# Kernel tuning notes

Measured on AMD Instinct MI355X. Metric: run time of the kernel, lower is better.

## Reference

```python
import jax, jax.numpy as jnp
import numpy as np

B, N, D, QM, QP, NP, T = 16, 900, 256, 4, 4, 6, 4


def setup_inputs() -> dict:
    key = jax.random.key(0)
    ks = jax.random.split(key, 12)
    return {
        "motion_query": jax.random.normal(ks[0], (B, N, D), jnp.float32),
        "plan_query": jax.random.normal(ks[1], (B, NP, D), jnp.float32),
        "ego_status_feature": jax.random.normal(ks[2], (B, D), jnp.float32),
        "motion_queue": jax.random.normal(ks[3], (B, QM, N, D), jnp.float32),
        "plan_queue": jax.random.normal(ks[4], (B, QP, NP, D), jnp.float32),
        "ego_status_queue": jax.random.normal(ks[5], (B, QP, D), jnp.float32),
        "period": jax.random.randint(ks[6], (B, QM), 0, 4, jnp.int32),
        "mask": jax.random.bernoulli(ks[7], 0.9, (B,)),
        "temp_anchor_embed_forstate": jax.random.normal(ks[8], (B, N, T, D), jnp.float32),
        "temp_mask_forstate": jax.random.bernoulli(ks[9], 0.5, (B, N, T)),
        "ego_temp_anchor_embed_forstate": jax.random.normal(ks[10], (B, 1, T, D), jnp.float32),
        "ego_temp_mask_forstate": jax.random.bernoulli(ks[11], 0.5, (B, 1, T)),
    }


def reference(motion_query, plan_query, ego_status_feature, motion_queue,
              plan_queue, ego_status_queue, period, mask,
              temp_anchor_embed_forstate, temp_mask_forstate,
              ego_temp_anchor_embed_forstate, ego_temp_mask_forstate):
    sg = jax.lax.stop_gradient
    # --- masked queue reset: for batch rows with mask==False, overwrite every
    # queue entry with the (detached) current value and zero the period ---
    reset = ~mask  # [B]
    mq = jnp.where(reset[:, None, None, None], sg(motion_query)[:, None], motion_queue)
    pq = jnp.where(reset[:, None, None, None], sg(plan_query)[:, None], plan_queue)
    eq = jnp.where(reset[:, None, None], sg(ego_status_feature)[:, None], ego_status_queue)
    per = jnp.where(reset[:, None], 0, period)

    # --- temporal window: T == 4, so both branches take the simple slice ---
    mm = temp_mask_forstate[..., :-1]            # [B, N, T-1]
    me = temp_anchor_embed_forstate[..., :-1, :]  # [B, N, T-1, D]
    pm = ego_temp_mask_forstate[..., :-1]         # [B, 1, T-1]
    pe = ego_temp_anchor_embed_forstate[..., :-1, :]  # [B, 1, T-1, D]

    # --- propagate plan embed forward over masked prefix ---
    any_flag = jnp.any(pm)
    all_true = jnp.all(pm, axis=(-2, -1))                # [B]
    m1 = pm[:, 0, :]                                     # [B, T-1] (Np == 1)
    first_false = jnp.argmin(m1, axis=-1)                # [B] index of first False
    Tm1 = pm.shape[-1]
    # embed at first-False slot (else branch) vs last-frame ego embed (all-True)
    repl_else = jnp.take_along_axis(pe, first_false[:, None, None, None], axis=2)[:, :, 0, :]
    repl_all = ego_temp_anchor_embed_forstate[:, :, -1, :]
    repl = jnp.where(all_true[:, None, None], repl_all, repl_else)  # [B, 1, D]
    j = jnp.arange(Tm1)
    overwrite = all_true[:, None] | (j[None, :] < first_false[:, None])  # [B, T-1]
    pe = jnp.where(any_flag & overwrite[:, None, :, None], repl[:, :, None, :], pe)

    return (mq, pq, eq, per,
            mm.swapaxes(1, 2), me.swapaxes(1, 2),
            pm.swapaxes(1, 2), pe.swapaxes(1, 2))
```

## Files before the change

### kernel.cpp

```cpp
#include <hip/hip_runtime.h>
#include <stdint.h>

namespace {
constexpr int Bn = 16, Nn = 900, Dn = 256, QMn = 4, QPn = 4, NPn = 6, Tn = 4;

constexpr int SZ_MQ  = Bn * QMn * Nn * Dn;
constexpr int SZ_PQ  = Bn * QPn * NPn * Dn;
constexpr int SZ_EQ  = Bn * QPn * Dn;
constexpr int SZ_PER = Bn * QMn;
constexpr int SZ_MM  = Bn * (Tn - 1) * Nn;
constexpr int SZ_ME  = Bn * (Tn - 1) * Nn * Dn;
constexpr int SZ_PM  = Bn * (Tn - 1);
constexpr int SZ_PE  = Bn * (Tn - 1) * Dn;

constexpr int OFF_MQ  = 0;
constexpr int OFF_PQ  = OFF_MQ + SZ_MQ;
constexpr int OFF_EQ  = OFF_PQ + SZ_PQ;
constexpr int OFF_PER = OFF_EQ + SZ_EQ;
constexpr int OFF_MM  = OFF_PER + SZ_PER;
constexpr int OFF_ME  = OFF_MM + SZ_MM;
constexpr int OFF_PM  = OFF_ME + SZ_ME;
constexpr int OFF_PE  = OFF_PM + SZ_PM;
constexpr int TOTAL   = OFF_PE + SZ_PE;
}

using u16 = unsigned short;

__device__ __forceinline__ float bits_to_f(unsigned u) {
    return __builtin_bit_cast(float, u);
}

__device__ int detect_float_mode(const void* p) {
    const unsigned* w = (const unsigned*)p;
    int cnt = 0;
#pragma unroll
    for (int i = 0; i < 32; ++i) {
        unsigned ex = (w[i] >> 7) & 0xFFu;
        cnt += (ex >= 120u && ex <= 133u) ? 1 : 0;
    }
    return (cnt >= 16) ? 1 : 0;
}

enum { BM_I32 = 0, BM_U8 = 1, BM_BF16 = 2, BM_F32 = 3 };
__device__ int detect_bool_mode(const void* p) {
    const unsigned* w = (const unsigned*)p;
    unsigned orw = 0, or_even = 0;
    bool hw_ok = true, u8_ok = true;
#pragma unroll
    for (int i = 0; i < 64; ++i) {
        unsigned x = w[i];
        orw |= x;
        unsigned lo = x & 0xFFFFu, hi = x >> 16;
        hw_ok = hw_ok && (lo == 0u || lo == 0x3F80u) && (hi == 0u || hi == 0x3F80u);
        or_even |= lo;
        u8_ok = u8_ok && ((x & 0xFEFEFEFEu) == 0u);
    }
    if (orw <= 1u) return BM_I32;
    if (hw_ok)     return (or_even == 0u) ? BM_F32 : BM_BF16;
    if (u8_ok)     return BM_U8;
    return BM_I32;
}

__device__ __forceinline__ bool get_bool(const void* p, int i, int m) {
    if (m == BM_I32) return ((const int*)p)[i] != 0;
    if (m == BM_U8)  return ((const unsigned char*)p)[i] != 0;
    if (m == BM_BF16) return ((const u16*)p)[i] != 0;
    return ((const unsigned*)p)[i] != 0;
}

__device__ int detect_period_mode(const void* p) {
    const unsigned* w = (const unsigned*)p;
    unsigned orw = 0, or_even = 0;
    bool hw_ok = true;
#pragma unroll
    for (int i = 0; i < 16; ++i) {
        unsigned x = w[i];
        orw |= x;
        unsigned lo = x & 0xFFFFu, hi = x >> 16;
        bool lo_ok = (lo == 0u || lo == 0x3F80u || lo == 0x4000u || lo == 0x4040u);
        bool hi_ok = (hi == 0u || hi == 0x3F80u || hi == 0x4000u || hi == 0x4040u);
        hw_ok = hw_ok && lo_ok && hi_ok;
        or_even |= lo;
    }
    if (orw <= 3u) return 0;
    if (hw_ok && or_even == 0u) return 2;
    return 1;
}

__device__ __forceinline__ float get_period_f(const void* p, int i, int m) {
    if (m == 0) return (float)((const int*)p)[i];
    if (m == 1) return bits_to_f((unsigned)((const u16*)p)[i] << 16);
    return ((const float*)p)[i];
}

__device__ __forceinline__ void load8f(const void* base, int e, int fm,
                                       float4& A, float4& B) {
    if (fm == 0) {
        const float* f = (const float*)base + e;
        A = reinterpret_cast<const float4*>(f)[0];
        B = reinterpret_cast<const float4*>(f)[1];
    } else {
        const int4 r = *reinterpret_cast<const int4*>((const u16*)base + e);
        unsigned x;
        x = (unsigned)r.x; A.x = bits_to_f(x << 16); A.y = bits_to_f(x & 0xFFFF0000u);
        x = (unsigned)r.y; A.z = bits_to_f(x << 16); A.w = bits_to_f(x & 0xFFFF0000u);
        x = (unsigned)r.z; B.x = bits_to_f(x << 16); B.y = bits_to_f(x & 0xFFFF0000u);
        x = (unsigned)r.w; B.z = bits_to_f(x << 16); B.w = bits_to_f(x & 0xFFFF0000u);
    }
}

__global__ __launch_bounds__(256) void state_queue_kernel(
    const void* __restrict__ motion_query,
    const void* __restrict__ plan_query,
    const void* __restrict__ ego_status_feature,
    const void* __restrict__ motion_queue,
    const void* __restrict__ plan_queue,
    const void* __restrict__ ego_status_queue,
    const void* __restrict__ period,
    const void* __restrict__ mask,
    const void* __restrict__ temp_anchor,
    const void* __restrict__ temp_mask,
    const void* __restrict__ ego_anchor,
    const void* __restrict__ ego_mask,
    float* __restrict__ out)
{
    __shared__ int s_modes[3];
    if (threadIdx.x == 0) {
        s_modes[0] = detect_float_mode(motion_query);
        s_modes[1] = detect_bool_mode(temp_mask);
        s_modes[2] = detect_period_mode(period);
    }
    __syncthreads();
    const int fm = s_modes[0];
    const int bm = s_modes[1];
    const int pmode = s_modes[2];

    const int pack = blockIdx.x * blockDim.x + threadIdx.x;
    const int idx = pack * 8;
    if (idx >= TOTAL) return;

    float4 A, B;

    if (idx < OFF_PQ) {
        const int e = idx - OFF_MQ;
        const int d = e & (Dn - 1);
        const unsigned row = (unsigned)(e >> 8);
        const unsigned bq = row / (unsigned)Nn;
        const unsigned n = row - bq * (unsigned)Nn;
        const unsigned b = bq >> 2;
        const bool reset = !get_bool(mask, (int)b, bm);
        if (reset) load8f(motion_query, (((int)b * Nn + (int)n) << 8) + d, fm, A, B);
        else       load8f(motion_queue, e, fm, A, B);
    } else if (idx < OFF_EQ) {
        const int e = idx - OFF_PQ;
        const int d = e & (Dn - 1);
        const unsigned row = (unsigned)(e >> 8);
        const unsigned b = row / (unsigned)(QPn * NPn);
        const unsigned rem = row - b * (unsigned)(QPn * NPn);
        const unsigned q = rem / (unsigned)NPn;
        const unsigned p = rem - q * (unsigned)NPn;
        const bool reset = !get_bool(mask, (int)b, bm);
        if (reset) load8f(plan_query, (((int)b * NPn + (int)p) << 8) + d, fm, A, B);
        else       load8f(plan_queue, e, fm, A, B);
    } else if (idx < OFF_PER) {
        const int e = idx - OFF_EQ;
        const int d = e & (Dn - 1);
        const int row = e >> 8;
        const int b = row >> 2;
        const bool reset = !get_bool(mask, b, bm);
        if (reset) load8f(ego_status_feature, (b << 8) + d, fm, A, B);
        else       load8f(ego_status_queue, e, fm, A, B);
    } else if (idx < OFF_MM) {
        const int e = idx - OFF_PER;
        float h[8];
#pragma unroll
        for (int k = 0; k < 8; ++k) {
            const int g = e + k;
            const int b = g >> 2;
            const bool reset = !get_bool(mask, b, bm);
            h[k] = reset ? 0.0f : get_period_f(period, g, pmode);
        }
        A = make_float4(h[0], h[1], h[2], h[3]);
        B = make_float4(h[4], h[5], h[6], h[7]);
    } else if (idx < OFF_ME) {
        const int e = idx - OFF_MM;
        float h[8];
#pragma unroll
        for (int k = 0; k < 8; ++k) {
            const unsigned g = (unsigned)(e + k);
            const unsigned b = g / (unsigned)((Tn - 1) * Nn);
            const unsigned rem = g - b * (unsigned)((Tn - 1) * Nn);
            const unsigned t = rem / (unsigned)Nn;
            const unsigned n = rem - t * (unsigned)Nn;
            h[k] = get_bool(temp_mask, ((int)b * Nn + (int)n) * Tn + (int)t, bm)
                       ? 1.0f : 0.0f;
        }
        A = make_float4(h[0], h[1], h[2], h[3]);
        B = make_float4(h[4], h[5], h[6], h[7]);
    } else if (idx < OFF_PM) {
        const int e = idx - OFF_ME;
        const int d = e & (Dn - 1);
        const unsigned row = (unsigned)(e >> 8);
        const unsigned b = row / (unsigned)((Tn - 1) * Nn);
        const unsigned rem = row - b * (unsigned)((Tn - 1) * Nn);
        const unsigned t = rem / (unsigned)Nn;
        const unsigned n = rem - t * (unsigned)Nn;
        load8f(temp_anchor, ((((int)b * Nn + (int)n) * Tn + (int)t) << 8) + d, fm, A, B);
    } else if (idx < OFF_PE) {
        const int e = idx - OFF_PM;
        float h[8];
#pragma unroll
        for (int k = 0; k < 8; ++k) {
            const unsigned g = (unsigned)(e + k);
            const unsigned b = g / (unsigned)(Tn - 1);
            const unsigned t = g - b * (unsigned)(Tn - 1);
            h[k] = get_bool(ego_mask, (int)b * Tn + (int)t, bm) ? 1.0f : 0.0f;
        }
        A = make_float4(h[0], h[1], h[2], h[3]);
        B = make_float4(h[4], h[5], h[6], h[7]);
    } else {
        const int e = idx - OFF_PE;
        const int d = e & (Dn - 1);
        const unsigned row = (unsigned)(e >> 8);
        const unsigned b = row / (unsigned)(Tn - 1);
        const unsigned t = row - b * (unsigned)(Tn - 1);

        bool any_flag = false;
#pragma unroll
        for (int bb = 0; bb < Bn; ++bb) {
            any_flag = any_flag || get_bool(ego_mask, bb * Tn + 0, bm)
                                || get_bool(ego_mask, bb * Tn + 1, bm)
                                || get_bool(ego_mask, bb * Tn + 2, bm);
        }

        const bool p0 = get_bool(ego_mask, (int)b * Tn + 0, bm);
        const bool p1 = get_bool(ego_mask, (int)b * Tn + 1, bm);
        const bool p2 = get_bool(ego_mask, (int)b * Tn + 2, bm);
        const bool all_true = p0 && p1 && p2;
        const int first_false = (!p0) ? 0 : ((!p1) ? 1 : ((!p2) ? 2 : 0));

        const bool overwrite = all_true || ((int)t < first_false);
        int src_t = (int)t;
        if (any_flag && overwrite) src_t = all_true ? (Tn - 1) : first_false;

        load8f(ego_anchor, (((int)b * Tn + src_t) << 8) + d, fm, A, B);
    }

    reinterpret_cast<float4*>(out + idx)[0] = A;
    reinterpret_cast<float4*>(out + idx)[1] = B;
}

extern "C" void kernel_launch(void* const* d_in, const int* in_sizes, int n_in,
                              void* d_out, int out_size, void* d_ws, size_t ws_size,
                              hipStream_t stream) {
    float* out = (float*)d_out;
    const int packs = TOTAL / 8;
    const int threads = 256;
    const int blocks = (packs + threads - 1) / threads;
    state_queue_kernel<<<blocks, threads, 0, stream>>>(
        d_in[0], d_in[1], d_in[2], d_in[3], d_in[4], d_in[5], d_in[6], d_in[7],
        d_in[8], d_in[9], d_in[10], d_in[11], out);
}
```

Before: 219.1 us.

## Use persistent grid-stride loop with 4x unrolled loads and nontemporal stores

After: 231.9 us. 1.06x slower.

```diff
diff --git a/kernel.cpp b/kernel.cpp
--- a/kernel.cpp
+++ b/kernel.cpp
@@ -22,9 +22,11 @@
 constexpr int OFF_PM  = OFF_ME + SZ_ME;
 constexpr int OFF_PE  = OFF_PM + SZ_PM;
 constexpr int TOTAL   = OFF_PE + SZ_PE;
+constexpr int NPACKS  = TOTAL / 8;
 }
 
 using u16 = unsigned short;
+typedef float f32x4 __attribute__((ext_vector_type(4)));
 
 __device__ __forceinline__ float bits_to_f(unsigned u) {
     return __builtin_bit_cast(float, u);
@@ -107,6 +109,137 @@
         x = (unsigned)r.z; B.x = bits_to_f(x << 16); B.y = bits_to_f(x & 0xFFFF0000u);
         x = (unsigned)r.w; B.z = bits_to_f(x << 16); B.w = bits_to_f(x & 0xFFFF0000u);
     }
+}
+
+__device__ __forceinline__ void compute_pack(
+    int pack, int fm, int bm, int pmode,
+    const void* __restrict__ motion_query,
+    const void* __restrict__ plan_query,
+    const void* __restrict__ ego_status_feature,
+    const void* __restrict__ motion_queue,
+    const void* __restrict__ plan_queue,
+    const void* __restrict__ ego_status_queue,
+    const void* __restrict__ period,
+    const void* __restrict__ mask,
+    const void* __restrict__ temp_anchor,
+    const void* __restrict__ temp_mask,
+    const void* __restrict__ ego_anchor,
+    const void* __restrict__ ego_mask,
+    float4& A, float4& B)
+{
+    const int idx = pack * 8;
+
+    if (idx < OFF_PQ) {
+        const int e = idx - OFF_MQ;
+        const int d = e & (Dn - 1);
+        const unsigned row = (unsigned)(e >> 8);
+        const unsigned bq = row / (unsigned)Nn;
+        const unsigned n = row - bq * (unsigned)Nn;
+        const unsigned b = bq >> 2;
+        const bool reset = !get_bool(mask, (int)b, bm);
+        if (reset) load8f(motion_query, (((int)b * Nn + (int)n) << 8) + d, fm, A, B);
+        else       load8f(motion_queue, e, fm, A, B);
+    } else if (idx < OFF_EQ) {
+        const int e = idx - OFF_PQ;
+        const int d = e & (Dn - 1);
+        const unsigned row = (unsigned)(e >> 8);
+        const unsigned b = row / (unsigned)(QPn * NPn);
+        const unsigned rem = row - b * (unsigned)(QPn * NPn);
+        const unsigned q = rem / (unsigned)NPn;
+        const unsigned p = rem - q * (unsigned)NPn;
+        const bool reset = !get_bool(mask, (int)b, bm);
+        if (reset) load8f(plan_query, (((int)b * NPn + (int)p) << 8) + d, fm, A, B);
+        else       load8f(plan_queue, e, fm, A, B);
+    } else if (idx < OFF_PER) {
+        const int e = idx - OFF_EQ;
+        const int d = e & (Dn - 1);
+        const int row = e >> 8;
+        const int b = row >> 2;
+        const bool reset = !get_bool(mask, b, bm);
+        if (reset) load8f(ego_status_feature, (b << 8) + d, fm, A, B);
+        else       load8f(ego_status_queue, e, fm, A, B);
+    } else if (idx < OFF_MM) {
+        const int e = idx - OFF_PER;
+        float h[8];
+#pragma unroll
+        for (int k = 0; k < 8; ++k) {
+            const int g = e + k;
+            const int b = g >> 2;
+            const bool reset = !get_bool(mask, b, bm);
+            h[k] = reset ? 0.0f : get_period_f(period, g, pmode);
+        }
+        A = make_float4(h[0], h[1], h[2], h[3]);
+        B = make_float4(h[4], h[5], h[6], h[7]);
+    } else if (idx < OFF_ME) {
+        const int e = idx - OFF_MM;
+        float h[8];
+#pragma unroll
+        for (int k = 0; k < 8; ++k) {
+            const unsigned g = (unsigned)(e + k);
+            const unsigned b = g / (unsigned)((Tn - 1) * Nn);
+            const unsigned rem = g - b * (unsigned)((Tn - 1) * Nn);
+            const unsigned t = rem / (unsigned)Nn;
+            const unsigned n = rem - t * (unsigned)Nn;
+            h[k] = get_bool(temp_mask, ((int)b * Nn + (int)n) * Tn + (int)t, bm)
+                       ? 1.0f : 0.0f;
+        }
+        A = make_float4(h[0], h[1], h[2], h[3]);
+        B = make_float4(h[4], h[5], h[6], h[7]);
+    } else if (idx < OFF_PM) {
+        const int e = idx - OFF_ME;
+        const int d = e & (Dn - 1);
+        const unsigned row = (unsigned)(e >> 8);
+        const unsigned b = row / (unsigned)((Tn - 1) * Nn);
+        const unsigned rem = row - b * (unsigned)((Tn - 1) * Nn);
+        const unsigned t = rem / (unsigned)Nn;
+        const unsigned n = rem - t * (unsigned)Nn;
+        load8f(temp_anchor, ((((int)b * Nn + (int)n) * Tn + (int)t) << 8) + d, fm, A, B);
+    } else if (idx < OFF_PE) {
+        const int e = idx - OFF_PM;
+        float h[8];
+#pragma unroll
+        for (int k = 0; k < 8; ++k) {
+            const unsigned g = (unsigned)(e + k);
+            const unsigned b = g / (unsigned)(Tn - 1);
+            const unsigned t = g - b * (unsigned)(Tn - 1);
+            h[k] = get_bool(ego_mask, (int)b * Tn + (int)t, bm) ? 1.0f : 0.0f;
+        }
+        A = make_float4(h[0], h[1], h[2], h[3]);
+        B = make_float4(h[4], h[5], h[6], h[7]);
+    } else {
+        const int e = idx - OFF_PE;
+        const int d = e & (Dn - 1);
+        const unsigned row = (unsigned)(e >> 8);
+        const unsigned b = row / (unsigned)(Tn - 1);
+        const unsigned t = row - b * (unsigned)(Tn - 1);
+
+        bool any_flag = false;
+#pragma unroll
+        for (int bb = 0; bb < Bn; ++bb) {
+            any_flag = any_flag || get_bool(ego_mask, bb * Tn + 0, bm)
+                                || get_bool(ego_mask, bb * Tn + 1, bm)
+                                || get_bool(ego_mask, bb * Tn + 2, bm);
+        }
+
+        const bool p0 = get_bool(ego_mask, (int)b * Tn + 0, bm);
+        const bool p1 = get_bool(ego_mask, (int)b * Tn + 1, bm);
+        const bool p2 = get_bool(ego_mask, (int)b * Tn + 2, bm);
+        const bool all_true = p0 && p1 && p2;
+        const int first_false = (!p0) ? 0 : ((!p1) ? 1 : ((!p2) ? 2 : 0));
+
+        const bool overwrite = all_true || ((int)t < first_false);
+        int src_t = (int)t;
+        if (any_flag && overwrite) src_t = all_true ? (Tn - 1) : first_false;
+
+        load8f(ego_anchor, (((int)b * Tn + src_t) << 8) + d, fm, A, B);
+    }
+}
+
+__device__ __forceinline__ void store_pack_nt(float* __restrict__ out, int pack,
+                                              const float4& A, const float4& B) {
+    f32x4* p = reinterpret_cast<f32x4*>(out + pack * 8);
+    __builtin_nontemporal_store(__builtin_bit_cast(f32x4, A), p);
+    __builtin_nontemporal_store(__builtin_bit_cast(f32x4, B), p + 1);
 }
 
 __global__ __launch_bounds__(256) void state_queue_kernel(
@@ -135,128 +268,48 @@
     const int bm = s_modes[1];
     const int pmode = s_modes[2];
 
-    const int pack = blockIdx.x * blockDim.x + threadIdx.x;
-    const int idx = pack * 8;
-    if (idx >= TOTAL) return;
-
-    float4 A, B;
-
-    if (idx < OFF_PQ) {
-        const int e = idx - OFF_MQ;
-        const int d = e & (Dn - 1);
-        const unsigned row = (unsigned)(e >> 8);
-        const unsigned bq = row / (unsigned)Nn;
-        const unsigned n = row - bq * (unsigned)Nn;
-        const unsigned b = bq >> 2;
-        const bool reset = !get_bool(mask, (int)b, bm);
-        if (reset) load8f(motion_query, (((int)b * Nn + (int)n) << 8) + d, fm, A, B);
-        else       load8f(motion_queue, e, fm, A, B);
-    } else if (idx < OFF_EQ) {
-        const int e = idx - OFF_PQ;
-        const int d = e & (Dn - 1);
-        const unsigned row = (unsigned)(e >> 8);
-        const unsigned b = row / (unsigned)(QPn * NPn);
-        const unsigned rem = row - b * (unsigned)(QPn * NPn);
-        const unsigned q = rem / (unsigned)NPn;
-        const unsigned p = rem - q * (unsigned)NPn;
-        const bool reset = !get_bool(mask, (int)b, bm);
-        if (reset) load8f(plan_query, (((int)b * NPn + (int)p) << 8) + d, fm, A, B);
-        else       load8f(plan_queue, e, fm, A, B);
-    } else if (idx < OFF_PER) {
-        const int e = idx - OFF_EQ;
-        const int d = e & (Dn - 1);
-        const int row = e >> 8;
-        const int b = row >> 2;
-        const bool reset = !get_bool(mask, b, bm);
-        if (reset) load8f(ego_status_feature, (b << 8) + d, fm, A, B);
-        else       load8f(ego_status_queue, e, fm, A, B);
-    } else if (idx < OFF_MM) {
-        const int e = idx - OFF_PER;
-        float h[8];
-#pragma unroll
-        for (int k = 0; k < 8; ++k) {
-            const int g = e + k;
-            const int b = g >> 2;
-            const bool reset = !get_bool(mask, b, bm);
-            h[k] = reset ? 0.0f : get_period_f(period, g, pmode);
-        }
-        A = make_float4(h[0], h[1], h[2], h[3]);
-        B = make_float4(h[4], h[5], h[6], h[7]);
-    } else if (idx < OFF_ME) {
-        const int e = idx - OFF_MM;
-        float h[8];
-#pragma unroll
-        for (int k = 0; k < 8; ++k) {
-            const unsigned g = (unsigned)(e + k);
-            const unsigned b = g / (unsigned)((Tn - 1) * Nn);
-            const unsigned rem = g - b * (unsigned)((Tn - 1) * Nn);
-            const unsigned t = rem / (unsigned)Nn;
-            const unsigned n = rem - t * (unsigned)Nn;
-            h[k] = get_bool(temp_mask, ((int)b * Nn + (int)n) * Tn + (int)t, bm)
-                       ? 1.0f : 0.0f;
-        }
-        A = make_float4(h[0], h[1], h[2], h[3]);
-        B = make_float4(h[4], h[5], h[6], h[7]);
-    } else if (idx < OFF_PM) {
-        const int e = idx - OFF_ME;
-        const int d = e & (Dn - 1);
-        const unsigned row = (unsigned)(e >> 8);
-        const unsigned b = row / (unsigned)((Tn - 1) * Nn);
-        const unsigned rem = row - b * (unsigned)((Tn - 1) * Nn);
-        const unsigned t = rem / (unsigned)Nn;
-        const unsigned n = rem - t * (unsigned)Nn;
-        load8f(temp_anchor, ((((int)b * Nn + (int)n) * Tn + (int)t) << 8) + d, fm, A, B);
-    } else if (idx < OFF_PE) {
-        const int e = idx - OFF_PM;
-        float h[8];
-#pragma unroll
-        for (int k = 0; k < 8; ++k) {
-            const unsigned g = (unsigned)(e + k);
-            const unsigned b = g / (unsigned)(Tn - 1);
-            const unsigned t = g - b * (unsigned)(Tn - 1);
-            h[k] = get_bool(ego_mask, (int)b * Tn + (int)t, bm) ? 1.0f : 0.0f;
-        }
-        A = make_float4(h[0], h[1], h[2], h[3]);
-        B = make_float4(h[4], h[5], h[6], h[7]);
-    } else {
-        const int e = idx - OFF_PE;
-        const int d = e & (Dn - 1);
-        const unsigned row = (unsigned)(e >> 8);
-        const unsigned b = row / (unsigned)(Tn - 1);
-        const unsigned t = row - b * (unsigned)(Tn - 1);
-
-        bool any_flag = false;
-#pragma unroll
-        for (int bb = 0; bb < Bn; ++bb) {
-            any_flag = any_flag || get_bool(ego_mask, bb * Tn + 0, bm)
-                                || get_bool(ego_mask, bb * Tn + 1, bm)
-                                || get_bool(ego_mask, bb * Tn + 2, bm);
-        }
-
-        const bool p0 = get_bool(ego_mask, (int)b * Tn + 0, bm);
-        const bool p1 = get_bool(ego_mask, (int)b * Tn + 1, bm);
-        const bool p2 = get_bool(ego_mask, (int)b * Tn + 2, bm);
-        const bool all_true = p0 && p1 && p2;
-        const int first_false = (!p0) ? 0 : ((!p1) ? 1 : ((!p2) ? 2 : 0));
-
-        const bool overwrite = all_true || ((int)t < first_false);
-        int src_t = (int)t;
-        if (any_flag && overwrite) src_t = all_true ? (Tn - 1) : first_false;
-
-        load8f(ego_anchor, (((int)b * Tn + src_t) << 8) + d, fm, A, B);
-    }
-
-    reinterpret_cast<float4*>(out + idx)[0] = A;
-    reinterpret_cast<float4*>(out + idx)[1] = B;
+    const int stride = (int)(gridDim.x * blockDim.x);
+    int pack = (int)(blockIdx.x * blockDim.x + threadIdx.x);
+
+    for (; pack + 3 * stride < NPACKS; pack += 4 * stride) {
+        float4 A0, B0, A1, B1, A2, B2, A3, B3;
+        compute_pack(pack + 0 * stride, fm, bm, pmode,
+                     motion_query, plan_query, ego_status_feature, motion_queue,
+                     plan_queue, ego_status_queue, period, mask, temp_anchor,
+                     temp_mask, ego_anchor, ego_mask, A0, B0);
+        compute_pack(pack + 1 * stride, fm, bm, pmode,
+                     motion_query, plan_query, ego_status_feature, motion_queue,
+                     plan_queue, ego_status_queue, period, mask, temp_anchor,
+                     temp_mask, ego_anchor, ego_mask, A1, B1);
+        compute_pack(pack + 2 * stride, fm, bm, pmode,
+                     motion_query, plan_query, ego_status_feature, motion_queue,
+                     plan_queue, ego_status_queue, period, mask, temp_anchor,
+                     temp_mask, ego_anchor, ego_mask, A2, B2);
+        compute_pack(pack + 3 * stride, fm, bm, pmode,
+                     motion_query, plan_query, ego_status_feature, motion_queue,
+                     plan_queue, ego_status_queue, period, mask, temp_anchor,
+                     temp_mask, ego_anchor, ego_mask, A3, B3);
+        store_pack_nt(out, pack + 0 * stride, A0, B0);
+        store_pack_nt(out, pack + 1 * stride, A1, B1);
+        store_pack_nt(out, pack + 2 * stride, A2, B2);
+        store_pack_nt(out, pack + 3 * stride, A3, B3);
+    }
+    for (; pack < NPACKS; pack += stride) {
+        float4 A, B;
+        compute_pack(pack, fm, bm, pmode,
+                     motion_query, plan_query, ego_status_feature, motion_queue,
+                     plan_queue, ego_status_queue, period, mask, temp_anchor,
+                     temp_mask, ego_anchor, ego_mask, A, B);
+        store_pack_nt(out, pack, A, B);
+    }
 }
 
 extern "C" void kernel_launch(void* const* d_in, const int* in_sizes, int n_in,
                               void* d_out, int out_size, void* d_ws, size_t ws_size,
                               hipStream_t stream) {
     float* out = (float*)d_out;
-    const int packs = TOTAL / 8;
     const int threads = 256;
-    const int blocks = (packs + threads - 1) / threads;
+    const int blocks = 1024;
     state_queue_kernel<<<blocks, threads, 0, stream>>>(
         d_in[0], d_in[1], d_in[2], d_in[3], d_in[4], d_in[5], d_in[6], d_in[7],
         d_in[8], d_in[9], d_in[10], d_in[11], out);
```
